# Kernel tuning notes

Hardware: AMD Instinct MI355X
Metric: run time of the kernel (lower is better)

Reference implementation:

```python
import jax, jax.numpy as jnp
import numpy as np

H = 256           # lstm_hidden_dim
D_IN = 22         # input_dim
H1, H2, H3 = 1024, 512, 1024
RRI = 2
N_R = N_L = 384


def _lstm_dir(x, Wih, Whh, b, reverse):
    # x: [T, D]; Wih: [4H, D]; Whh: [4H, H]; b: [4H] (bih+bhh). PyTorch gate order i,f,g,o.
    xs = x[::-1] if reverse else x
    pre = xs @ Wih.T + b                       # [T, 4H] input projection hoisted out of scan
    hdim = Whh.shape[1]

    def step(carry, p):
        h, c = carry
        g = p + h @ Whh.T
        i, f, gg, o = jnp.split(g, 4)
        i = jax.nn.sigmoid(i); f = jax.nn.sigmoid(f)
        gg = jnp.tanh(gg); o = jax.nn.sigmoid(o)
        c = f * c + i * gg
        h = o * jnp.tanh(c)
        return (h, c), h

    h0 = jnp.zeros((hdim,), x.dtype)
    _, hs = jax.lax.scan(step, (h0, h0), pre)
    return hs[::-1] if reverse else hs


def _bilstm(x, Wih0, Whh0, bih0, bhh0, Wih1, Whh1, bih1, bhh1):
    # 2-layer bidirectional LSTM (dropout between layers is identity in eval).
    b0 = bih0 + bhh0
    x1 = jnp.concatenate([_lstm_dir(x, Wih0[0], Whh0[0], b0[0], False),
                          _lstm_dir(x, Wih0[1], Whh0[1], b0[1], True)], axis=-1)
    b1 = bih1 + bhh1
    return jnp.concatenate([_lstm_dir(x1, Wih1[0], Whh1[0], b1[0], False),
                            _lstm_dir(x1, Wih1[1], Whh1[1], b1[1], True)], axis=-1)


def _mlp(h, W1, b1, W2, b2):
    h1 = jax.nn.relu(h @ W1.T + b1)
    return jax.nn.relu(h1 @ W2.T + b2)   # [N, H2]


def setup_inputs() -> dict:
    key = jax.random.key(0)
    ks = jax.random.split(key, 20)
    s = 0.05
    f = lambda k, shp: (jax.random.normal(k, shp, dtype=jnp.float32) * s)
    return {
        "v_r": jax.random.normal(ks[0], (N_R, D_IN), dtype=jnp.float32),
        "v_l": jax.random.normal(ks[1], (N_L, D_IN), dtype=jnp.float32),
        # LSTM layer 0 (input D_IN), stacked over 2 directions
        "Wih0": f(ks[2], (2, 4 * H, D_IN)),
        "Whh0": f(ks[3], (2, 4 * H, H)),
        "bih0": f(ks[4], (2, 4 * H)),
        "bhh0": f(ks[5], (2, 4 * H)),
        # LSTM layer 1 (input 2H)
        "Wih1": f(ks[6], (2, 4 * H, 2 * H)),
        "Whh1": f(ks[7], (2, 4 * H, H)),
        "bih1": f(ks[8], (2, 4 * H)),
        "bhh1": f(ks[9], (2, 4 * H)),
        # MLP heads
        "W1": f(ks[10], (H1, 2 * H)), "b1": f(ks[11], (H1,)),
        "W2": f(ks[12], (H2, H1)),    "b2": f(ks[13], (H2,)),
        "W3": f(ks[14], (H3, 2 * H2)), "b3": f(ks[15], (H3,)),
        "Wout": f(ks[16], (RRI, H3)), "bout": f(ks[17], (RRI,)),
    }


def reference(v_r, v_l, Wih0, Whh0, bih0, bhh0, Wih1, Whh1, bih1, bhh1,
              W1, b1, W2, b2, W3, b3, Wout, bout):
    out_r = _bilstm(v_r, Wih0, Whh0, bih0, bhh0, Wih1, Whh1, bih1, bhh1)  # [Nr, 2H]
    out_l = _bilstm(v_l, Wih0, Whh0, bih0, bhh0, Wih1, Whh1, bih1, bhh1)  # [Nl, 2H]
    hr = _mlp(out_r, W1, b1, W2, b2)   # [Nr, H2]
    hl = _mlp(out_l, W1, b1, W2, b2)   # [Nl, H2]
    # Original: 0.5*(Linear3([hr_i, hl_j]) + Linear3([hl_j, hr_i])) built via huge
    # repeat()s; exactly equal to u_r[i] + u_l[j] + b3 with the split weight sum.
    d2 = hr.shape[-1]
    W3s = (W3[:, :d2] + W3[:, d2:]).T            # [H2, H3]
    u_r = 0.5 * (hr @ W3s)                       # [Nr, H3]
    u_l = 0.5 * (hl @ W3s)                       # [Nl, H3]
    conv = jax.nn.relu(u_r[:, None, :] + u_l[None, :, :] + b3)  # [Nr, Nl, H3]
    v_in = conv.reshape(-1, conv.shape[-1])      # [Nr*Nl, H3], i_r-major like the torch loop
    logits = v_in @ Wout.T + bout                # [Nr*Nl, rri_size]
    return jax.nn.log_softmax(logits, axis=-1)
```

## Files before the change

### kernel.cpp

```cpp
#include <hip/hip_runtime.h>
#include <math.h>


typedef _Float16 half2_t __attribute__((ext_vector_type(2)));

__device__ __forceinline__ float fast_sig(float x) {
    float e = __expf(-x);
    return __builtin_amdgcn_rcpf(1.f + e);
}
__device__ __forceinline__ float fast_tanh(float x) {
    x = fminf(fmaxf(x, -30.f), 30.f);
    float e = __expf(2.f * x);
    return (e - 1.f) * __builtin_amdgcn_rcpf(e + 1.f);
}

__global__ __launch_bounds__(256) void prep_kernel(
    const float* __restrict__ bih0, const float* __restrict__ bhh0,
    const float* __restrict__ bih1, const float* __restrict__ bhh1,
    const float* __restrict__ W3,   const float* __restrict__ Wout,
    float* __restrict__ b0sum, float* __restrict__ b1sum,
    float* __restrict__ W3sum, float* __restrict__ woutT)
{
    int idx = blockIdx.x * 256 + threadIdx.x;
    int stride = gridDim.x * 256;
    if (idx < 2048) {
        b0sum[idx] = bih0[idx] + bhh0[idx];
        b1sum[idx] = bih1[idx] + bhh1[idx];
        woutT[idx] = Wout[(idx & 1) * 1024 + (idx >> 1)];
    }
    for (int i = idx; i < 1024 * 512; i += stride) {
        int n = i >> 9, k = i & 511;
        W3sum[i] = W3[n * 1024 + k] + W3[n * 1024 + 512 + k];
    }
}

__global__ __launch_bounds__(256) void proj0_kernel(
    const float* __restrict__ v_r, const float* __restrict__ v_l,
    const float* __restrict__ Wih0, const float* __restrict__ b0sum,
    float* __restrict__ pre0)
{
    int t = blockIdx.x;
    int sd = blockIdx.y;
    int seq = sd >> 1, dir = sd & 1;
    const float* x = (seq ? v_l : v_r) + t * 22;
    __shared__ float sx[22];
    if (threadIdx.x < 22) sx[threadIdx.x] = x[threadIdx.x];
    __syncthreads();
#pragma unroll
    for (int q = 0; q < 4; ++q) {
        int o = q * 256 + threadIdx.x;
        const float* wr = Wih0 + (size_t)(dir * 1024 + o) * 22;
        float acc = b0sum[dir * 1024 + o];
#pragma unroll
        for (int d = 0; d < 22; ++d) acc += sx[d] * wr[d];
        pre0[((size_t)sd * 384 + t) * 1024 + o] = acc;
    }
}

__global__ __launch_bounds__(512, 2) void lstm_rec_kernel(
    const float* __restrict__ Whh,
    const float* __restrict__ pre,
    float* __restrict__ out,
    unsigned long long* pub,
    int layer)
{
    const int b = blockIdx.x;
    const int chain = b & 7;
    const int w = b >> 3;
    if (chain >= 4) return;
    const int seq = chain >> 1, dir = chain & 1;
    const int tid = threadIdx.x;
    const int ks = tid & 3;
    const int r = tid >> 2;
    const int j = (w << 7) + r;
    const int wp = 1 - w;

    __shared__ __align__(16) half2_t hh[2][128];

    float wto[4][16], wtr[4][16];
#pragma unroll
    for (int g = 0; g < 4; ++g) {
        const float* wrow = Whh + (((size_t)(dir * 1024 + g * 256 + j)) << 8);
        const float* po = wrow + (w << 7) + (ks << 5);
        const float* pr = wrow + (wp << 7) + (ks << 5);
#pragma unroll
        for (int q = 0; q < 16; ++q) {
            float2 vo = *(const float2*)(po + 2 * q);
            float2 vr = *(const float2*)(pr + 2 * q);
            half2_t ho2; ho2.x = (_Float16)vo.x; ho2.y = (_Float16)vo.y;
            half2_t hr2; hr2.x = (_Float16)vr.x; hr2.y = (_Float16)vr.y;
            wto[g][q] = __builtin_bit_cast(float, ho2);
            wtr[g][q] = __builtin_bit_cast(float, hr2);
        }
    }
#pragma unroll
    for (int g = 0; g < 4; ++g)
#pragma unroll
        for (int q = 0; q < 16; ++q)
            asm volatile("" : "+v"(wto[g][q]), "+v"(wtr[g][q]));

    if (tid < 128) {
        hh[0][tid] = half2_t{(_Float16)0.f, (_Float16)0.f};
        hh[1][tid] = half2_t{(_Float16)0.f, (_Float16)0.f};
    }
    float cstate = 0.f;

    const bool isPub  = (ks == 0) && ((r & 1) == 0);
    const bool isOut  = (ks == 1);
    const bool isPoll = (ks == 3) && ((r & 1) == 1);
    const int  p  = r >> 1;
    __syncthreads();

    for (int s = 0; s < 384; ++s) {
        const int t = dir ? (383 - s) : s;
        const float* pre_t = (layer == 0)
            ? pre + ((size_t)(seq * 2 + dir) * 384 + t) * 1024
            : pre + (((size_t)(seq * 384 + t)) * 2 + dir) * 1024;
        float pv = pre_t[(ks << 8) + j];

        const int par = s & 1;
        float a0 = 0.f, a1 = 0.f, a2 = 0.f, a3 = 0.f;
        {
            const float4* ro = (const float4*)&hh[par][(w << 6) + (ks << 4)];
            float4 ho[4];
#pragma unroll
            for (int m = 0; m < 4; ++m) ho[m] = ro[m];
#pragma unroll
            for (int m = 0; m < 4; ++m) {
                const float he[4] = {ho[m].x, ho[m].y, ho[m].z, ho[m].w};
#pragma unroll
                for (int e = 0; e < 4; ++e) {
                    half2_t hv = __builtin_bit_cast(half2_t, he[e]);
                    int q = 4 * m + e;
                    a0 = __builtin_amdgcn_fdot2(__builtin_bit_cast(half2_t, wto[0][q]), hv, a0, false);
                    a1 = __builtin_amdgcn_fdot2(__builtin_bit_cast(half2_t, wto[1][q]), hv, a1, false);
                    a2 = __builtin_amdgcn_fdot2(__builtin_bit_cast(half2_t, wto[2][q]), hv, a2, false);
                    a3 = __builtin_amdgcn_fdot2(__builtin_bit_cast(half2_t, wto[3][q]), hv, a3, false);
                }
            }
        }
        if (isPoll && s > 0) {
            unsigned long long* pb = pub + ((size_t)chain * 2 + par) * 128;
            const unsigned long long* src = &pb[(wp << 6) + p];
            const unsigned expect = (unsigned)s;
            unsigned long long v =
                __hip_atomic_load(src, __ATOMIC_RELAXED, __HIP_MEMORY_SCOPE_AGENT);
            if ((unsigned)(v >> 32) != expect) {
                for (int it = 0; it < 65536; ++it) {
                    __builtin_amdgcn_s_sleep(1);
                    v = __hip_atomic_load(src, __ATOMIC_RELAXED, __HIP_MEMORY_SCOPE_AGENT);
                    if ((unsigned)(v >> 32) == expect) break;
                }
            }
            hh[par][(wp << 6) + p] = __builtin_bit_cast(half2_t, (unsigned)v);
        }
        __syncthreads();

        {
            const float4* rr = (const float4*)&hh[par][(wp << 6) + (ks << 4)];
            float4 hr[4];
#pragma unroll
            for (int m = 0; m < 4; ++m) hr[m] = rr[m];
#pragma unroll
            for (int m = 0; m < 4; ++m) {
                const float he[4] = {hr[m].x, hr[m].y, hr[m].z, hr[m].w};
#pragma unroll
                for (int e = 0; e < 4; ++e) {
                    half2_t hv = __builtin_bit_cast(half2_t, he[e]);
                    int q = 4 * m + e;
                    a0 = __builtin_amdgcn_fdot2(__builtin_bit_cast(half2_t, wtr[0][q]), hv, a0, false);
                    a1 = __builtin_amdgcn_fdot2(__builtin_bit_cast(half2_t, wtr[1][q]), hv, a1, false);
                    a2 = __builtin_amdgcn_fdot2(__builtin_bit_cast(half2_t, wtr[2][q]), hv, a2, false);
                    a3 = __builtin_amdgcn_fdot2(__builtin_bit_cast(half2_t, wtr[3][q]), hv, a3, false);
                }
            }
        }
        a0 += (ks == 0) ? pv : 0.f;
        a1 += (ks == 1) ? pv : 0.f;
        a2 += (ks == 2) ? pv : 0.f;
        a3 += (ks == 3) ? pv : 0.f;
#pragma unroll
        for (int d = 1; d < 4; d <<= 1) {
            a0 += __shfl_xor(a0, d);
            a1 += __shfl_xor(a1, d);
            a2 += __shfl_xor(a2, d);
            a3 += __shfl_xor(a3, d);
        }

        float iv = fast_sig(a0);
        float fv = fast_sig(a1);
        float gv = fast_tanh(a2);
        float ov = fast_sig(a3);
        cstate = fv * cstate + iv * gv;
        float h = ov * fast_tanh(cstate);

        unsigned hb = (unsigned)__builtin_bit_cast(unsigned short, (_Float16)h);
        unsigned nb = (unsigned)__shfl_xor((int)hb, 4);
        const int pn = par ^ 1;
        if (isPub) {
            unsigned payload = (hb & 0xffffu) | (nb << 16);
            int P = (w << 6) + p;
            hh[pn][P] = __builtin_bit_cast(half2_t, payload);
            unsigned long long pk =
                ((unsigned long long)(unsigned)(s + 1) << 32) | payload;
            __hip_atomic_store(&pub[((size_t)chain * 2 + pn) * 128 + P], pk,
                               __ATOMIC_RELAXED, __HIP_MEMORY_SCOPE_AGENT);
        }
        if (isOut) {
            out[((size_t)seq * 384 + t) * 512 + dir * 256 + j] = h;
        }
        __syncthreads();
    }
}

__global__ __launch_bounds__(256) void gemm_nt_kernel(
    const float* __restrict__ A, const float* __restrict__ W,
    const float* __restrict__ bias, float* __restrict__ C,
    int M, int N, int K, float scale, int do_relu)
{
    __shared__ float As[32][68];
    __shared__ float Ws[32][68];
    const int tid = threadIdx.x;
    const int n0 = blockIdx.x * 64, m0 = blockIdx.y * 64;
    const int lr = tid >> 2;
    const int lk = (tid & 3) * 8;
    const int tm = tid >> 4, tn = tid & 15;
    float acc[4][4];
#pragma unroll
    for (int i = 0; i < 4; ++i)
#pragma unroll
        for (int j = 0; j < 4; ++j) acc[i][j] = 0.f;

    for (int kc = 0; kc < K; kc += 32) {
        float4 a0 = *(const float4*)(A + (size_t)(m0 + lr) * K + kc + lk);
        float4 a1 = *(const float4*)(A + (size_t)(m0 + lr) * K + kc + lk + 4);
        float4 w0 = *(const float4*)(W + (size_t)(n0 + lr) * K + kc + lk);
        float4 w1 = *(const float4*)(W + (size_t)(n0 + lr) * K + kc + lk + 4);
        __syncthreads();
        As[lk + 0][lr] = a0.x; As[lk + 1][lr] = a0.y; As[lk + 2][lr] = a0.z; As[lk + 3][lr] = a0.w;
        As[lk + 4][lr] = a1.x; As[lk + 5][lr] = a1.y; As[lk + 6][lr] = a1.z; As[lk + 7][lr] = a1.w;
        Ws[lk + 0][lr] = w0.x; Ws[lk + 1][lr] = w0.y; Ws[lk + 2][lr] = w0.z; Ws[lk + 3][lr] = w0.w;
        Ws[lk + 4][lr] = w1.x; Ws[lk + 5][lr] = w1.y; Ws[lk + 6][lr] = w1.z; Ws[lk + 7][lr] = w1.w;
        __syncthreads();
#pragma unroll
        for (int kk = 0; kk < 32; ++kk) {
            float4 av = *(const float4*)&As[kk][tm * 4];
            float4 wv = *(const float4*)&Ws[kk][tn * 4];
            acc[0][0] += av.x * wv.x; acc[0][1] += av.x * wv.y; acc[0][2] += av.x * wv.z; acc[0][3] += av.x * wv.w;
            acc[1][0] += av.y * wv.x; acc[1][1] += av.y * wv.y; acc[1][2] += av.y * wv.z; acc[1][3] += av.y * wv.w;
            acc[2][0] += av.z * wv.x; acc[2][1] += av.z * wv.y; acc[2][2] += av.z * wv.z; acc[2][3] += av.z * wv.w;
            acc[3][0] += av.w * wv.x; acc[3][1] += av.w * wv.y; acc[3][2] += av.w * wv.z; acc[3][3] += av.w * wv.w;
        }
    }
    float4 bv = make_float4(0.f, 0.f, 0.f, 0.f);
    if (bias) bv = *(const float4*)(bias + n0 + tn * 4);
#pragma unroll
    for (int i = 0; i < 4; ++i) {
        int m = m0 + tm * 4 + i;
        float4 v;
        v.x = scale * acc[i][0] + bv.x;
        v.y = scale * acc[i][1] + bv.y;
        v.z = scale * acc[i][2] + bv.z;
        v.w = scale * acc[i][3] + bv.w;
        if (do_relu) {
            v.x = fmaxf(v.x, 0.f); v.y = fmaxf(v.y, 0.f);
            v.z = fmaxf(v.z, 0.f); v.w = fmaxf(v.w, 0.f);
        }
        *(float4*)(C + (size_t)m * N + n0 + tn * 4) = v;
    }
}

__global__ __launch_bounds__(256) void pairwise_kernel(
    const float* __restrict__ u,
    const float* __restrict__ woutT,
    const float* __restrict__ bout,
    float* __restrict__ out)
{
    __shared__ float Ur[32][132];
    __shared__ float Ul[32][132];
    __shared__ float Wo[256];
    const int tid = threadIdx.x;
    const int j0 = blockIdx.x * 32, i0 = blockIdx.y * 32;
    const int ii = tid >> 4, jj = tid & 15;
    const int il0 = ii, il1 = ii + 16;
    const int jl0 = jj, jl1 = jj + 16;
    float acc000 = 0.f, acc001 = 0.f, acc010 = 0.f, acc011 = 0.f;
    float acc100 = 0.f, acc101 = 0.f, acc110 = 0.f, acc111 = 0.f;
    const int lrw = tid >> 3;
    const int lcb = (tid & 7) * 16;

    for (int cc = 0; cc < 1024; cc += 128) {
        __syncthreads();
#pragma unroll
        for (int q = 0; q < 4; ++q) {
            *(float4*)&Ur[lrw][lcb + 4 * q] =
                *(const float4*)(u + (size_t)(i0 + lrw) * 1024 + cc + lcb + 4 * q);
            *(float4*)&Ul[lrw][lcb + 4 * q] =
                *(const float4*)(u + (size_t)(384 + j0 + lrw) * 1024 + cc + lcb + 4 * q);
        }
        if (tid < 128)
            *(float2*)&Wo[tid * 2] = *(const float2*)(woutT + (size_t)(cc + tid) * 2);
        __syncthreads();

        for (int c = 0; c < 128; c += 4) {
            float4 a0  = *(const float4*)&Ur[il0][c];
            float4 a1  = *(const float4*)&Ur[il1][c];
            float4 b0v = *(const float4*)&Ul[jl0][c];
            float4 b1v = *(const float4*)&Ul[jl1][c];
            float4 wA4 = *(const float4*)&Wo[c * 2];
            float4 wB4 = *(const float4*)&Wo[c * 2 + 4];
#define PW_STEP(AX, W0, W1)                                   \
            { float rr;                                       \
              rr = fmaxf(a0.AX + b0v.AX, 0.f); acc000 += rr*(W0); acc001 += rr*(W1); \
              rr = fmaxf(a0.AX + b1v.AX, 0.f); acc010 += rr*(W0); acc011 += rr*(W1); \
              rr = fmaxf(a1.AX + b0v.AX, 0.f); acc100 += rr*(W0); acc101 += rr*(W1); \
              rr = fmaxf(a1.AX + b1v.AX, 0.f); acc110 += rr*(W0); acc111 += rr*(W1); }
            PW_STEP(x, wA4.x, wA4.y)
            PW_STEP(y, wA4.z, wA4.w)
            PW_STEP(z, wB4.x, wB4.y)
            PW_STEP(w, wB4.z, wB4.w)
#undef PW_STEP
        }
    }
    float2 bo = *(const float2*)bout;
    float pa[2][2][2] = {{{acc000, acc001}, {acc010, acc011}},
                         {{acc100, acc101}, {acc110, acc111}}};
#pragma unroll
    for (int pi = 0; pi < 2; ++pi)
#pragma unroll
        for (int pj = 0; pj < 2; ++pj) {
            float l0 = pa[pi][pj][0] + bo.x;
            float l1 = pa[pi][pj][1] + bo.y;
            float m = fmaxf(l0, l1);
            float lse = m + logf(expf(l0 - m) + expf(l1 - m));
            int ig = i0 + ii + 16 * pi;
            int jg = j0 + jj + 16 * pj;
            float2 o2; o2.x = l0 - lse; o2.y = l1 - lse;
            *(float2*)(out + ((size_t)ig * 384 + jg) * 2) = o2;
        }
}

extern "C" void kernel_launch(void* const* d_in, const int* in_sizes, int n_in,
                              void* d_out, int out_size, void* d_ws, size_t ws_size,
                              hipStream_t stream)
{
    const float* v_r  = (const float*)d_in[0];
    const float* v_l  = (const float*)d_in[1];
    const float* Wih0 = (const float*)d_in[2];
    const float* Whh0 = (const float*)d_in[3];
    const float* bih0 = (const float*)d_in[4];
    const float* bhh0 = (const float*)d_in[5];
    const float* Wih1 = (const float*)d_in[6];
    const float* Whh1 = (const float*)d_in[7];
    const float* bih1 = (const float*)d_in[8];
    const float* bhh1 = (const float*)d_in[9];
    const float* W1   = (const float*)d_in[10];
    const float* b1   = (const float*)d_in[11];
    const float* W2   = (const float*)d_in[12];
    const float* b2   = (const float*)d_in[13];
    const float* W3   = (const float*)d_in[14];
    const float* b3   = (const float*)d_in[15];
    const float* Wout = (const float*)d_in[16];
    const float* bout = (const float*)d_in[17];
    float* out = (float*)d_out;

    float* ws = (float*)d_ws;
    size_t off = 0;
    float* b0sum = ws + off; off += 2048;
    float* b1sum = ws + off; off += 2048;
    float* W3sum = ws + off; off += 1024 * 512;
    float* woutT = ws + off; off += 2048;
    float* pre0  = ws + off; off += (size_t)4 * 384 * 1024;
    float* out0  = ws + off; off += (size_t)2 * 384 * 512;
    float* pre1  = ws + off; off += (size_t)768 * 2048;
    float* out1  = ws + off; off += (size_t)2 * 384 * 512;
    float* h1    = ws + off; off += (size_t)768 * 1024;
    float* h2    = ws + off; off += (size_t)768 * 512;
    float* u     = ws + off; off += (size_t)768 * 1024;
    unsigned long long* pub0 = (unsigned long long*)(ws + off); off += 4 * 2 * 128 * 2;
    unsigned long long* pub1 = (unsigned long long*)(ws + off); off += 4 * 2 * 128 * 2;

    prep_kernel<<<512, 256, 0, stream>>>(bih0, bhh0, bih1, bhh1, W3, Wout,
                                         b0sum, b1sum, W3sum, woutT);
    proj0_kernel<<<dim3(384, 4), 256, 0, stream>>>(v_r, v_l, Wih0, b0sum, pre0);
    lstm_rec_kernel<<<16, 512, 0, stream>>>(Whh0, pre0, out0, pub0, 0);
    gemm_nt_kernel<<<dim3(2048 / 64, 768 / 64), 256, 0, stream>>>(
        out0, Wih1, b1sum, pre1, 768, 2048, 512, 1.f, 0);
    lstm_rec_kernel<<<16, 512, 0, stream>>>(Whh1, pre1, out1, pub1, 1);
    gemm_nt_kernel<<<dim3(1024 / 64, 768 / 64), 256, 0, stream>>>(
        out1, W1, b1, h1, 768, 1024, 512, 1.f, 1);
    gemm_nt_kernel<<<dim3(512 / 64, 768 / 64), 256, 0, stream>>>(
        h1, W2, b2, h2, 768, 512, 1024, 1.f, 1);
    gemm_nt_kernel<<<dim3(1024 / 64, 384 / 64), 256, 0, stream>>>(
        h2, W3sum, b3, u, 384, 1024, 512, 0.5f, 0);
    gemm_nt_kernel<<<dim3(1024 / 64, 384 / 64), 256, 0, stream>>>(
        h2 + (size_t)384 * 512, W3sum, nullptr, u + (size_t)384 * 1024, 384, 1024, 512, 0.5f, 0);
    pairwise_kernel<<<dim3(12, 12), 256, 0, stream>>>(u, woutT, bout, out);
}
```

Baseline: 1.395 ms.

## Move remote-half recurrent weights from registers to shared memory

The LSTM recurrence kernel now keeps only the local half of its fp16 Whh slice in registers. The remote-half weights are staged once into a 128KB shared-memory buffer and read back every step. The launch-bounds minimum-blocks hint is dropped, so the compiler is no longer forced to fit two 512-thread blocks per CU, and register pressure falls. In exchange, every step adds LDS reads for weights on the critical path of the serial recurrence. The publish write to shared h is also reordered slightly.

```diff
diff --git a/kernel.cpp b/kernel.cpp
--- a/kernel.cpp
+++ b/kernel.cpp
@@ -57,7 +57,7 @@
     }
 }
 
-__global__ __launch_bounds__(512, 2) void lstm_rec_kernel(
+__global__ __launch_bounds__(512) void lstm_rec_kernel(
     const float* __restrict__ Whh,
     const float* __restrict__ pre,
     float* __restrict__ out,
@@ -71,44 +71,48 @@
     const int seq = chain >> 1, dir = chain & 1;
     const int tid = threadIdx.x;
     const int ks = tid & 3;
-    const int r = tid >> 2;
-    const int j = (w << 7) + r;
+    const int jloc = tid >> 2;
+    const int jj = (w << 7) + jloc;
     const int wp = 1 - w;
 
+    __shared__ __align__(16) float4 wl[16][512];
     __shared__ __align__(16) half2_t hh[2][128];
 
-    float wto[4][16], wtr[4][16];
-#pragma unroll
-    for (int g = 0; g < 4; ++g) {
-        const float* wrow = Whh + (((size_t)(dir * 1024 + g * 256 + j)) << 8);
-        const float* po = wrow + (w << 7) + (ks << 5);
-        const float* pr = wrow + (wp << 7) + (ks << 5);
-#pragma unroll
-        for (int q = 0; q < 16; ++q) {
-            float2 vo = *(const float2*)(po + 2 * q);
-            float2 vr = *(const float2*)(pr + 2 * q);
-            half2_t ho2; ho2.x = (_Float16)vo.x; ho2.y = (_Float16)vo.y;
-            half2_t hr2; hr2.x = (_Float16)vr.x; hr2.y = (_Float16)vr.y;
-            wto[g][q] = __builtin_bit_cast(float, ho2);
-            wtr[g][q] = __builtin_bit_cast(float, hr2);
-        }
-    }
-#pragma unroll
-    for (int g = 0; g < 4; ++g)
-#pragma unroll
-        for (int q = 0; q < 16; ++q)
-            asm volatile("" : "+v"(wto[g][q]), "+v"(wtr[g][q]));
-
-    if (tid < 128) {
-        hh[0][tid] = half2_t{(_Float16)0.f, (_Float16)0.f};
-        hh[1][tid] = half2_t{(_Float16)0.f, (_Float16)0.f};
-    }
+    float wA[64];
+    {
+#pragma unroll
+        for (int g = 0; g < 4; ++g) {
+            const float* wr = Whh + (((size_t)(dir * 1024 + g * 256 + jj)) << 8);
+            const float* po = wr + (w << 7) + (ks << 5);
+            const float* pr = wr + (wp << 7) + (ks << 5);
+#pragma unroll
+            for (int q = 0; q < 16; ++q) {
+                float2 v = *(const float2*)(po + 2 * q);
+                half2_t h2; h2.x = (_Float16)v.x; h2.y = (_Float16)v.y;
+                wA[g * 16 + q] = __builtin_bit_cast(float, h2);
+            }
+            for (int cc = 0; cc < 4; ++cc) {
+                float4 pk; float* pf = (float*)&pk;
+#pragma unroll
+                for (int e = 0; e < 4; ++e) {
+                    float2 v = *(const float2*)(pr + 8 * cc + 2 * e);
+                    half2_t h2; h2.x = (_Float16)v.x; h2.y = (_Float16)v.y;
+                    pf[e] = __builtin_bit_cast(float, h2);
+                }
+                wl[g * 4 + cc][tid] = pk;
+            }
+        }
+    }
+#pragma unroll
+    for (int q = 0; q < 64; ++q) asm volatile("" : "+v"(wA[q]));
+
+    if (tid < 128) hh[0][tid] = half2_t{(_Float16)0.f, (_Float16)0.f};
     float cstate = 0.f;
 
-    const bool isPub  = (ks == 0) && ((r & 1) == 0);
+    const bool isPub  = (ks == 2) && ((jloc & 1) == 0);
     const bool isOut  = (ks == 1);
-    const bool isPoll = (ks == 3) && ((r & 1) == 1);
-    const int  p  = r >> 1;
+    const bool isPoll = (ks == 3) && ((jloc & 1) == 1);
+    const int  p  = jloc >> 1;
     __syncthreads();
 
     for (int s = 0; s < 384; ++s) {
@@ -116,27 +120,24 @@
         const float* pre_t = (layer == 0)
             ? pre + ((size_t)(seq * 2 + dir) * 384 + t) * 1024
             : pre + (((size_t)(seq * 384 + t)) * 2 + dir) * 1024;
-        float pv = pre_t[(ks << 8) + j];
+        float pv = pre_t[(ks << 8) + jj];
 
         const int par = s & 1;
+        const float4* hb = (const float4*)hh[par];
         float a0 = 0.f, a1 = 0.f, a2 = 0.f, a3 = 0.f;
-        {
-            const float4* ro = (const float4*)&hh[par][(w << 6) + (ks << 4)];
-            float4 ho[4];
-#pragma unroll
-            for (int m = 0; m < 4; ++m) ho[m] = ro[m];
-#pragma unroll
-            for (int m = 0; m < 4; ++m) {
-                const float he[4] = {ho[m].x, ho[m].y, ho[m].z, ho[m].w};
-#pragma unroll
-                for (int e = 0; e < 4; ++e) {
-                    half2_t hv = __builtin_bit_cast(half2_t, he[e]);
-                    int q = 4 * m + e;
-                    a0 = __builtin_amdgcn_fdot2(__builtin_bit_cast(half2_t, wto[0][q]), hv, a0, false);
-                    a1 = __builtin_amdgcn_fdot2(__builtin_bit_cast(half2_t, wto[1][q]), hv, a1, false);
-                    a2 = __builtin_amdgcn_fdot2(__builtin_bit_cast(half2_t, wto[2][q]), hv, a2, false);
-                    a3 = __builtin_amdgcn_fdot2(__builtin_bit_cast(half2_t, wto[3][q]), hv, a3, false);
-                }
+
+#pragma unroll
+        for (int m = 0; m < 4; ++m) {
+            float4 hv4 = hb[(w << 4) + (ks << 2) + m];
+            const float he[4] = {hv4.x, hv4.y, hv4.z, hv4.w};
+#pragma unroll
+            for (int e = 0; e < 4; ++e) {
+                half2_t hv = __builtin_bit_cast(half2_t, he[e]);
+                int q = 4 * m + e;
+                a0 = __builtin_amdgcn_fdot2(__builtin_bit_cast(half2_t, wA[q]),      hv, a0, false);
+                a1 = __builtin_amdgcn_fdot2(__builtin_bit_cast(half2_t, wA[16 + q]), hv, a1, false);
+                a2 = __builtin_amdgcn_fdot2(__builtin_bit_cast(half2_t, wA[32 + q]), hv, a2, false);
+                a3 = __builtin_amdgcn_fdot2(__builtin_bit_cast(half2_t, wA[48 + q]), hv, a3, false);
             }
         }
         if (isPoll && s > 0) {
@@ -156,25 +157,28 @@
         }
         __syncthreads();
 
-        {
-            const float4* rr = (const float4*)&hh[par][(wp << 6) + (ks << 4)];
-            float4 hr[4];
-#pragma unroll
-            for (int m = 0; m < 4; ++m) hr[m] = rr[m];
-#pragma unroll
-            for (int m = 0; m < 4; ++m) {
-                const float he[4] = {hr[m].x, hr[m].y, hr[m].z, hr[m].w};
-#pragma unroll
-                for (int e = 0; e < 4; ++e) {
-                    half2_t hv = __builtin_bit_cast(half2_t, he[e]);
-                    int q = 4 * m + e;
-                    a0 = __builtin_amdgcn_fdot2(__builtin_bit_cast(half2_t, wtr[0][q]), hv, a0, false);
-                    a1 = __builtin_amdgcn_fdot2(__builtin_bit_cast(half2_t, wtr[1][q]), hv, a1, false);
-                    a2 = __builtin_amdgcn_fdot2(__builtin_bit_cast(half2_t, wtr[2][q]), hv, a2, false);
-                    a3 = __builtin_amdgcn_fdot2(__builtin_bit_cast(half2_t, wtr[3][q]), hv, a3, false);
-                }
+#pragma unroll
+        for (int m = 0; m < 4; ++m) {
+            float4 hv4 = hb[(wp << 4) + (ks << 2) + m];
+            float4 w0 = wl[m][tid];
+            float4 w1 = wl[4 + m][tid];
+            float4 w2 = wl[8 + m][tid];
+            float4 w3 = wl[12 + m][tid];
+            const float he[4] = {hv4.x, hv4.y, hv4.z, hv4.w};
+            const float e0[4] = {w0.x, w0.y, w0.z, w0.w};
+            const float e1[4] = {w1.x, w1.y, w1.z, w1.w};
+            const float e2[4] = {w2.x, w2.y, w2.z, w2.w};
+            const float e3[4] = {w3.x, w3.y, w3.z, w3.w};
+#pragma unroll
+            for (int e = 0; e < 4; ++e) {
+                half2_t hv = __builtin_bit_cast(half2_t, he[e]);
+                a0 = __builtin_amdgcn_fdot2(__builtin_bit_cast(half2_t, e0[e]), hv, a0, false);
+                a1 = __builtin_amdgcn_fdot2(__builtin_bit_cast(half2_t, e1[e]), hv, a1, false);
+                a2 = __builtin_amdgcn_fdot2(__builtin_bit_cast(half2_t, e2[e]), hv, a2, false);
+                a3 = __builtin_amdgcn_fdot2(__builtin_bit_cast(half2_t, e3[e]), hv, a3, false);
             }
         }
+
         a0 += (ks == 0) ? pv : 0.f;
         a1 += (ks == 1) ? pv : 0.f;
         a2 += (ks == 2) ? pv : 0.f;
@@ -194,20 +198,22 @@
         cstate = fv * cstate + iv * gv;
         float h = ov * fast_tanh(cstate);
 
-        unsigned hb = (unsigned)__builtin_bit_cast(unsigned short, (_Float16)h);
-        unsigned nb = (unsigned)__shfl_xor((int)hb, 4);
+        unsigned hb16 = (unsigned)__builtin_bit_cast(unsigned short, (_Float16)h);
+        unsigned nb = (unsigned)__shfl_xor((int)hb16, 4);
         const int pn = par ^ 1;
+        if (ks == 0) {
+            ((unsigned short*)hh[pn])[jj] = (unsigned short)hb16;
+        }
+        if (isOut) {
+            out[((size_t)seq * 384 + t) * 512 + dir * 256 + jj] = h;
+        }
         if (isPub) {
-            unsigned payload = (hb & 0xffffu) | (nb << 16);
+            unsigned payload = (hb16 & 0xffffu) | (nb << 16);
             int P = (w << 6) + p;
-            hh[pn][P] = __builtin_bit_cast(half2_t, payload);
             unsigned long long pk =
                 ((unsigned long long)(unsigned)(s + 1) << 32) | payload;
             __hip_atomic_store(&pub[((size_t)chain * 2 + pn) * 128 + P], pk,
                                __ATOMIC_RELAXED, __HIP_MEMORY_SCOPE_AGENT);
-        }
-        if (isOut) {
-            out[((size_t)seq * 384 + t) * 512 + dir * 256 + j] = h;
         }
         __syncthreads();
     }
```

New measurement: 1.510 ms. +8.2%, slower.
